# Kernel optimization log

Measured on AMD Instinct MI355X. Metric: run time of the kernel, lower is better.

Reference implementation:

```python
import jax, jax.numpy as jnp
import numpy as np

N, E, H, G = 50000, 800000, 256, 50
CUTOFF = 10.0
PI = float(np.pi)
LOG2 = float(np.log(2.0))

def ssp(x):
    # ShiftedSoftplus: softplus(x) - log(2)
    return jax.nn.softplus(x) - LOG2

def setup_inputs() -> dict:
    key = jax.random.key(0)
    ks = jax.random.split(key, 16)
    def lin(kw, kb, fan_in, fan_out):
        s = float(np.sqrt(6.0 / (fan_in + fan_out)))  # xavier_uniform
        W = jax.random.uniform(kw, (fan_in, fan_out), minval=-s, maxval=s, dtype=jnp.float32)
        b = jnp.zeros((fan_out,), jnp.float32)
        return W, b
    h = jax.random.normal(ks[0], (N, H), dtype=jnp.float32)
    edge_index = jax.random.randint(ks[1], (2, E), 0, N, dtype=jnp.int64)
    edge_weight = jax.random.uniform(ks[2], (E,), dtype=jnp.float32) * CUTOFF
    edge_attr = jax.random.normal(ks[3], (E, G), dtype=jnp.float32)
    aw_W, aw_b = lin(ks[4], ks[5], H, H)   # atom_wise
    m1_W, m1_b = lin(ks[6], ks[7], G, H)   # mlp[0]
    m2_W, m2_b = lin(ks[8], ks[9], H, H)   # mlp[2] (num_filters == hidden)
    o1_W, o1_b = lin(ks[10], ks[11], H, H) # out[0]
    o2_W, o2_b = lin(ks[12], ks[13], H, H) # out[2]
    return {"h": h, "edge_index": edge_index, "edge_weight": edge_weight,
            "edge_attr": edge_attr, "aw_W": aw_W, "aw_b": aw_b,
            "m1_W": m1_W, "m1_b": m1_b, "m2_W": m2_W, "m2_b": m2_b,
            "o1_W": o1_W, "o1_b": o1_b, "o2_W": o2_W, "o2_b": o2_b}

def reference(h, edge_index, edge_weight, edge_attr,
              aw_W, aw_b, m1_W, m1_b, m2_W, m2_b,
              o1_W, o1_b, o2_W, o2_b):
    n_nodes = h.shape[0]
    # atom-wise linear
    h1 = h @ aw_W + aw_b                                   # [N, H]
    # cosine cutoff per edge
    C = 0.5 * (jnp.cos(edge_weight * (PI / CUTOFF)) + 1.0) # [E]
    # edge filter MLP on RBF features
    Wf = ssp(ssp(edge_attr @ m1_W + m1_b) @ m2_W + m2_b)   # [E, H]
    Wf = Wf * C[:, None]
    # CFConv: gather x_j, modulate, scatter-add to target nodes
    src, dst = edge_index[0], edge_index[1]
    msg = h1[src] * Wf                                     # [E, H]
    agg = jax.ops.segment_sum(msg, dst, num_segments=n_nodes)
    # output MLP
    out = ssp(agg @ o1_W + o1_b) @ o2_W + o2_b             # [N, H]
    return out
```

## Files before the change

### kernel.cpp

```cpp
#include <hip/hip_runtime.h>

#define N_NODES 50000
#define N_EDGES 800000

typedef __attribute__((ext_vector_type(8))) short bf16x8;
typedef __attribute__((ext_vector_type(4))) float f32x4;
typedef __attribute__((ext_vector_type(2))) float f32x2;
typedef __attribute__((ext_vector_type(4))) unsigned int u32x4;

__device__ __forceinline__ float bf2f(unsigned int u) {
  union { unsigned int u; float f; } c; c.u = (u & 0xffffu) << 16; return c.f;
}
__device__ __forceinline__ unsigned short f2bf(float f) {
  union { float f; unsigned int u; } c; c.f = f;
  return (unsigned short)((c.u + 0x8000u) >> 16);
}
__device__ __forceinline__ unsigned int pk_bf16(float lo, float hi) {
  unsigned int r;
  asm("v_cvt_pk_bf16_f32 %0, %1, %2" : "=v"(r) : "v"(lo), "v"(hi));
  return r;
}

#if __has_builtin(__builtin_amdgcn_exp2f) && __has_builtin(__builtin_amdgcn_logf)
__device__ __forceinline__ float sspf(float x) {
  const float e = __builtin_amdgcn_exp2f(fabsf(x) * -1.44269504088896f);
  const float l = __builtin_amdgcn_logf(1.0f + e);
  return fmaf(0.69314718055994531f, l, fmaxf(x, 0.0f) - 0.69314718055994531f);
}
#else
__device__ __forceinline__ float sspf(float x) {
  return fmaxf(x, 0.0f) + __logf(1.0f + __expf(-fabsf(x))) - 0.69314718055994531f;
}
#endif

__device__ __forceinline__ f32x4 MFMA(bf16x8 a, bf16x8 b, f32x4 c) {
  return __builtin_amdgcn_mfma_f32_16x16x32_bf16(a, b, c, 0, 0, 0);
}
__device__ __forceinline__ f32x4 f4bcast(float v) {
  f32x4 z = {v, v, v, v}; return z;
}

__device__ __forceinline__ bf16x8 cvt8pk(const float* __restrict__ p) {
  f32x4 x0 = *(const f32x4*)p;
  f32x4 x1 = *(const f32x4*)(p + 4);
  union { u32x4 u; bf16x8 v; } r;
  r.u[0] = pk_bf16(x0[0], x0[1]);
  r.u[1] = pk_bf16(x0[2], x0[3]);
  r.u[2] = pk_bf16(x1[0], x1[1]);
  r.u[3] = pk_bf16(x1[2], x1[3]);
  return r.v;
}

template<int ADT, int ACT, int ODT>
__global__ __launch_bounds__(512, 8) void gemm512(
    const void* __restrict__ Av, const unsigned short* __restrict__ Wt,
    const float* __restrict__ bias, void* __restrict__ Outv, int M)
{
  __shared__ unsigned short a_lds[64 * 256];
  const int m0  = (int)blockIdx.x * 64;
  const int tid = (int)threadIdx.x;

  {
    const int r   = tid >> 3;
    const int oc8 = tid & 7;
    int row = m0 + r;
    if (row >= M) row = M - 1;
    if (ADT == 1) {
      const float* ap = (const float*)Av + (size_t)row * 256 + oc8 * 32;
#pragma unroll
      for (int q = 0; q < 4; ++q) {
        const bf16x8 v = cvt8pk(ap + q * 8);
        const int byt = r * 512 + ((oc8 * 64 + q * 16) ^ ((r & 7) << 4));
        *(bf16x8*)((char*)a_lds + byt) = v;
      }
    } else {
      const unsigned short* ap =
          (const unsigned short*)Av + (size_t)row * 256 + oc8 * 32;
#pragma unroll
      for (int q = 0; q < 4; ++q) {
        const bf16x8 v = *(const bf16x8*)(ap + q * 8);
        const int byt = r * 512 + ((oc8 * 64 + q * 16) ^ ((r & 7) << 4));
        *(bf16x8*)((char*)a_lds + byt) = v;
      }
    }
  }
  __syncthreads();

  const int w  = tid >> 6, l = tid & 63, lr = l & 15, g = l >> 4;
  const int c0 = w * 32;
  const int P45 = (lr & 3) << 4;
  const int P6  = (lr & 4) << 4;
  const int alb = lr * 512 + ((g * 16) ^ P45);

  const float bs0 = bias[c0 + lr];
  const float bs1 = bias[c0 + 16 + lr];
  f32x4 acc[4][2];
#pragma unroll
  for (int a = 0; a < 4; ++a) {
    acc[a][0] = f4bcast(bs0);
    acc[a][1] = f4bcast(bs1);
  }

#pragma unroll
  for (int ks = 0; ks < 8; ++ks) {
    const int kb = ks * 32 + g * 8;
    const bf16x8 bfr0 = *(const bf16x8*)(Wt + (size_t)(c0 + lr) * 256 + kb);
    const bf16x8 bfr1 = *(const bf16x8*)(Wt + (size_t)(c0 + 16 + lr) * 256 + kb);
    const char* abase = (const char*)a_lds + (alb + ((ks * 64) ^ P6));
#pragma unroll
    for (int mf = 0; mf < 4; ++mf) {
      const bf16x8 af = *(const bf16x8*)(abase + mf * 8192);
      __builtin_amdgcn_s_setprio(1);
      acc[mf][0] = MFMA(af, bfr0, acc[mf][0]);
      acc[mf][1] = MFMA(af, bfr1, acc[mf][1]);
      __builtin_amdgcn_s_setprio(0);
    }
  }

#pragma unroll
  for (int nf = 0; nf < 2; ++nf) {
    const int col = c0 + nf * 16 + lr;
#pragma unroll
    for (int mf = 0; mf < 4; ++mf) {
#pragma unroll
      for (int i = 0; i < 4; ++i) {
        const int row = m0 + mf * 16 + g * 4 + i;
        if (row < M) {
          float x = acc[mf][nf][i];
          if (ACT) x = sspf(x);
          if (ODT == 0)
            ((unsigned short*)Outv)[(size_t)row * 256 + col] = f2bf(x);
          else
            ((float*)Outv)[(size_t)row * 256 + col] = x;
        }
      }
    }
  }
}

__global__ __launch_bounds__(256) void hist_dst(const int* __restrict__ eidx,
                                                int* __restrict__ cnt)
{
  const int e = (int)blockIdx.x * 256 + (int)threadIdx.x;
  atomicAdd(&cnt[eidx[N_EDGES + e]], 1);
}

__global__ __launch_bounds__(1024) void scan_cnt(const int* __restrict__ cnt,
                                                 int* __restrict__ cursor)
{
  __shared__ int part[1024];
  const int t = (int)threadIdx.x;
  const int base = t * 49;
  int s = 0;
#pragma unroll 7
  for (int j = 0; j < 49; ++j) {
    const int idx = base + j;
    if (idx < N_NODES) s += cnt[idx];
  }
  part[t] = s;
  __syncthreads();
  for (int off = 1; off < 1024; off <<= 1) {
    int v = 0;
    if (t >= off) v = part[t - off];
    __syncthreads();
    part[t] += v;
    __syncthreads();
  }
  int run = (t == 0) ? 0 : part[t - 1];
#pragma unroll 7
  for (int j = 0; j < 49; ++j) {
    const int idx = base + j;
    if (idx < N_NODES) { cursor[idx] = run; run += cnt[idx]; }
  }
}

__global__ __launch_bounds__(256) void scatter_perm(
    const int* __restrict__ eidx, const float* __restrict__ ew,
    int* __restrict__ cursor, int* __restrict__ perm,
    float* __restrict__ Cf, int* __restrict__ srcs, int* __restrict__ dsts)
{
  const int e = (int)blockIdx.x * 256 + (int)threadIdx.x;
  const int d = eidx[N_EDGES + e];
  const int pos = atomicAdd(&cursor[d], 1);
  perm[pos] = e;
  Cf[pos]   = 0.5f * (__cosf(ew[e] * 0.31415926535897931f) + 1.0f);
  srcs[pos] = eidx[e];
  dsts[pos] = d;
}

__global__ __launch_bounds__(512, 8) void edge_fused512(
    const float* __restrict__ eattr, const int* __restrict__ perm,
    const float* __restrict__ Cf,
    const int* __restrict__ srcs, const int* __restrict__ dsts,
    const unsigned short* __restrict__ m1t, const float* __restrict__ m1b,
    const unsigned short* __restrict__ m2t, const float* __restrict__ m2b,
    const unsigned short* __restrict__ h1, float* __restrict__ agg)
{
  __shared__ unsigned short t_lds[64 * 256];
  __shared__ float Cs[64];
  __shared__ int s_src[64];
  __shared__ int s_dst[65];
  unsigned short* ea_lds = t_lds;

  const int e0  = (int)blockIdx.x * 64;
  const int tid = (int)threadIdx.x;

  {
    const int r  = tid >> 3;
    const int oc = tid & 7;
    const int p  = perm[e0 + r];
    const float* ap = eattr + (size_t)p * 50 + oc * 8;
    union { u32x4 u; bf16x8 v; } t;
    if (oc < 6) {
      f32x2 a0 = *(const f32x2*)(ap);
      f32x2 a1 = *(const f32x2*)(ap + 2);
      f32x2 a2 = *(const f32x2*)(ap + 4);
      f32x2 a3 = *(const f32x2*)(ap + 6);
      t.u[0] = pk_bf16(a0[0], a0[1]);
      t.u[1] = pk_bf16(a1[0], a1[1]);
      t.u[2] = pk_bf16(a2[0], a2[1]);
      t.u[3] = pk_bf16(a3[0], a3[1]);
    } else if (oc == 6) {
      f32x2 a0 = *(const f32x2*)(ap);
      t.u[0] = pk_bf16(a0[0], a0[1]);
      t.u[1] = 0; t.u[2] = 0; t.u[3] = 0;
    } else {
      t.u[0] = 0; t.u[1] = 0; t.u[2] = 0; t.u[3] = 0;
    }
    const int byt = r * 128 + ((oc * 16) ^ ((r & 7) << 4));
    *(bf16x8*)((char*)ea_lds + byt) = t.v;
  }
  if (tid < 64) {
    Cs[tid]    = Cf[e0 + tid];
    s_src[tid] = srcs[e0 + tid];
    s_dst[tid] = dsts[e0 + tid];
  }
  if (tid == 64)
    s_dst[64] = (e0 + 64 < N_EDGES) ? dsts[e0 + 64] : -1;
  __syncthreads();

  const int w  = tid >> 6;
  const int l  = tid & 63;
  const int lr = l & 15;
  const int g  = l >> 4;
  const int c0 = w * 32;

  const int P45  = (lr & 3) << 4;
  const int P6   = (lr & 4) << 4;
  const int alb1 = lr * 128 + ((g * 16) ^ P45);
  const int alb2 = lr * 512 + ((g * 16) ^ P45);

  const float b10 = m1b[c0 + lr];
  const float b11 = m1b[c0 + 16 + lr];
  f32x4 acc[4][2];
#pragma unroll
  for (int a = 0; a < 4; ++a) {
    acc[a][0] = f4bcast(b10);
    acc[a][1] = f4bcast(b11);
  }

#pragma unroll
  for (int ks = 0; ks < 2; ++ks) {
    const int kb = ks * 32 + g * 8;
    const bf16x8 bfr0 = *(const bf16x8*)(m1t + (c0 + lr) * 64 + kb);
    const bf16x8 bfr1 = *(const bf16x8*)(m1t + (c0 + 16 + lr) * 64 + kb);
    const char* abase = (const char*)ea_lds + (alb1 + ((ks * 64) ^ P6));
#pragma unroll
    for (int mf = 0; mf < 4; ++mf) {
      const bf16x8 af = *(const bf16x8*)(abase + mf * 2048);
      __builtin_amdgcn_s_setprio(1);
      acc[mf][0] = MFMA(af, bfr0, acc[mf][0]);
      acc[mf][1] = MFMA(af, bfr1, acc[mf][1]);
      __builtin_amdgcn_s_setprio(0);
    }
  }
  __syncthreads();

#pragma unroll
  for (int nf = 0; nf < 2; ++nf) {
    const int colb = (c0 + nf * 16 + lr) * 2;
#pragma unroll
    for (int i = 0; i < 4; ++i) {
      const int gi = g * 4 + i;
      char* wp = (char*)t_lds + (gi * 512 + (colb ^ ((gi & 7) << 4)));
      const float v0 = sspf(acc[0][nf][i]);
      const float v1 = sspf(acc[1][nf][i]);
      const float v2 = sspf(acc[2][nf][i]);
      const float v3 = sspf(acc[3][nf][i]);
      const unsigned int p01 = pk_bf16(v0, v1);
      const unsigned int p23 = pk_bf16(v2, v3);
      *(unsigned short*)(wp)         = (unsigned short)p01;
      *(unsigned short*)(wp + 8192)  = (unsigned short)(p01 >> 16);
      *(unsigned short*)(wp + 16384) = (unsigned short)p23;
      *(unsigned short*)(wp + 24576) = (unsigned short)(p23 >> 16);
    }
  }
  __syncthreads();

  const float b20 = m2b[c0 + lr];
  const float b21 = m2b[c0 + 16 + lr];
#pragma unroll
  for (int a = 0; a < 4; ++a) {
    acc[a][0] = f4bcast(b20);
    acc[a][1] = f4bcast(b21);
  }

#pragma unroll
  for (int ks = 0; ks < 8; ++ks) {
    const int kb = ks * 32 + g * 8;
    const bf16x8 bfr0 = *(const bf16x8*)(m2t + (size_t)(c0 + lr) * 256 + kb);
    const bf16x8 bfr1 = *(const bf16x8*)(m2t + (size_t)(c0 + 16 + lr) * 256 + kb);
    const char* abase = (const char*)t_lds + (alb2 + ((ks * 64) ^ P6));
#pragma unroll
    for (int mf = 0; mf < 4; ++mf) {
      const bf16x8 af = *(const bf16x8*)(abase + mf * 8192);
      __builtin_amdgcn_s_setprio(1);
      acc[mf][0] = MFMA(af, bfr0, acc[mf][0]);
      acc[mf][1] = MFMA(af, bfr1, acc[mf][1]);
      __builtin_amdgcn_s_setprio(0);
    }
  }
  __syncthreads();

#pragma unroll
  for (int nf = 0; nf < 2; ++nf) {
    const int colb = (c0 + nf * 16 + lr) * 2;
#pragma unroll
    for (int i = 0; i < 4; ++i) {
      const int gi = g * 4 + i;
      char* wp = (char*)t_lds + (gi * 512 + (colb ^ ((gi & 7) << 4)));
      const float v0 = sspf(acc[0][nf][i]) * Cs[gi];
      const float v1 = sspf(acc[1][nf][i]) * Cs[16 + gi];
      const float v2 = sspf(acc[2][nf][i]) * Cs[32 + gi];
      const float v3 = sspf(acc[3][nf][i]) * Cs[48 + gi];
      const unsigned int p01 = pk_bf16(v0, v1);
      const unsigned int p23 = pk_bf16(v2, v3);
      *(unsigned short*)(wp)         = (unsigned short)p01;
      *(unsigned short*)(wp + 8192)  = (unsigned short)(p01 >> 16);
      *(unsigned short*)(wp + 16384) = (unsigned short)p23;
      *(unsigned short*)(wp + 24576) = (unsigned short)(p23 >> 16);
    }
  }
  __syncthreads();

  {
    const int q2 = tid >> 7;
    const int cp = (tid & 127) * 2;
    const int rb = q2 * 16;
    float s0 = 0.f, s1 = 0.f;
#pragma unroll
    for (int rr = 0; rr < 16; ++rr) {
      const int r = rb + rr;
      const int byt = r * 512 + ((cp * 2) ^ ((r & 7) << 4));
      const unsigned int wfp = *(const unsigned int*)((const char*)t_lds + byt);
      const unsigned int xjp =
          *(const unsigned int*)(h1 + (size_t)s_src[r] * 256 + cp);
      s0 += bf2f(wfp) * bf2f(xjp);
      s1 += bf2f(wfp >> 16) * bf2f(xjp >> 16);
      const int d = s_dst[r];
      if (rr == 15 || s_dst[r + 1] != d) {
        float* ap = agg + (size_t)d * 256 + cp;
        atomicAdd(ap, s0);
        atomicAdd(ap + 1, s1);
        s0 = 0.f; s1 = 0.f;
      }
    }
  }
}

__global__ __launch_bounds__(256) void prep_weights(
    const float* __restrict__ aw, const float* __restrict__ m1,
    const float* __restrict__ m2, const float* __restrict__ o1,
    const float* __restrict__ o2,
    unsigned short* __restrict__ awt, unsigned short* __restrict__ m1t,
    unsigned short* __restrict__ m2t, unsigned short* __restrict__ o1t,
    unsigned short* __restrict__ o2t)
{
  const int i = (int)blockIdx.x * 256 + (int)threadIdx.x;
  const int c = i >> 8, k = i & 255;
  const int src = k * 256 + c;
  awt[i] = f2bf(aw[src]);
  m2t[i] = f2bf(m2[src]);
  o1t[i] = f2bf(o1[src]);
  o2t[i] = f2bf(o2[src]);
  if (k < 64) m1t[c * 64 + k] = (k < 50) ? f2bf(m1[k * 256 + c]) : (unsigned short)0;
}

extern "C" void kernel_launch(void* const* d_in, const int* in_sizes, int n_in,
                              void* d_out, int out_size, void* d_ws, size_t ws_size,
                              hipStream_t stream)
{
  const float* h    = (const float*)d_in[0];
  const int*   eidx = (const int*)d_in[1];
  const float* ew   = (const float*)d_in[2];
  const float* ea   = (const float*)d_in[3];
  const float* awW  = (const float*)d_in[4];
  const float* awb  = (const float*)d_in[5];
  const float* m1W  = (const float*)d_in[6];
  const float* m1b  = (const float*)d_in[7];
  const float* m2W  = (const float*)d_in[8];
  const float* m2b  = (const float*)d_in[9];
  const float* o1W  = (const float*)d_in[10];
  const float* o1b  = (const float*)d_in[11];
  const float* o2W  = (const float*)d_in[12];
  const float* o2b  = (const float*)d_in[13];

  char* ws = (char*)d_ws;
  unsigned short* h1  = (unsigned short*)ws;
  float*          agg = (float*)(ws + 25600000);
  char* wbase = ws + 25600000 + 51200000;
  unsigned short* awt = (unsigned short*)wbase;
  unsigned short* m2t = awt + 65536;
  unsigned short* o1t = m2t + 65536;
  unsigned short* o2t = o1t + 65536;
  unsigned short* m1t = o2t + 65536;
  char* p0 = wbase + 4 * 131072 + 32768;
  int* cnt    = (int*)p0;
  int* cursor = cnt + N_NODES;
  int* perm   = cursor + N_NODES;
  char* p1 = p0 + 400000 + 3200000;
  float* Cf   = (float*)p1;
  int*   srcs = (int*)(p1 + 3200000);
  int*   dsts = (int*)(p1 + 6400000);

  hipMemsetAsync(agg, 0, (size_t)N_NODES * 256 * 4, stream);
  hipMemsetAsync(cnt, 0, (size_t)N_NODES * 4, stream);

  prep_weights<<<256, 256, 0, stream>>>(awW, m1W, m2W, o1W, o2W,
                                        awt, m1t, m2t, o1t, o2t);
  hist_dst<<<N_EDGES / 256, 256, 0, stream>>>(eidx, cnt);
  scan_cnt<<<1, 1024, 0, stream>>>(cnt, cursor);
  scatter_perm<<<N_EDGES / 256, 256, 0, stream>>>(eidx, ew, cursor, perm,
                                                  Cf, srcs, dsts);

  gemm512<1, 0, 0><<<(N_NODES + 63) / 64, 512, 0, stream>>>(h, awt, awb, h1, N_NODES);

  edge_fused512<<<N_EDGES / 64, 512, 0, stream>>>(
      ea, perm, Cf, srcs, dsts, m1t, m1b, m2t, m2b, h1, agg);

  gemm512<1, 1, 0><<<(N_NODES + 63) / 64, 512, 0, stream>>>(agg, o1t, o1b, h1, N_NODES);
  gemm512<0, 0, 1><<<(N_NODES + 63) / 64, 512, 0, stream>>>(h1, o2t, o2b, d_out, N_NODES);
}
```

Baseline: 698.6 us.

## Fuse output MLP GEMMs, prefetch gathered features, replace interior atomics with stores

Adds out_fused512, which runs both output linear layers in one kernel and keeps the SSP intermediate in LDS as bf16 instead of writing it to global memory. In the edge kernel, the h1 source-row gathers are issued before the barrier into registers so they overlap with the filter epilogue. Segment sums whose destination does not cross a 16-row group boundary are written with plain vector stores instead of atomics, since edges are sorted by destination. This relies on each destination's edges being contiguous and fully owned by one thread group; a destination spanning more than two groups could be written non-atomically and give wrong results.

New measurement: 813.1 us. 16.4% more time.

```diff
diff --git a/kernel.cpp b/kernel.cpp
--- a/kernel.cpp
+++ b/kernel.cpp
@@ -138,6 +138,126 @@
   }
 }
 
+__global__ __launch_bounds__(512, 8) void out_fused512(
+    const float* __restrict__ agg,
+    const unsigned short* __restrict__ o1t, const float* __restrict__ o1b,
+    const unsigned short* __restrict__ o2t, const float* __restrict__ o2b,
+    float* __restrict__ Out, int M)
+{
+  __shared__ unsigned short t_lds[64 * 256];
+  const int m0  = (int)blockIdx.x * 64;
+  const int tid = (int)threadIdx.x;
+
+  {
+    const int r   = tid >> 3;
+    const int oc8 = tid & 7;
+    int row = m0 + r;
+    if (row >= M) row = M - 1;
+    const float* ap = agg + (size_t)row * 256 + oc8 * 32;
+#pragma unroll
+    for (int q = 0; q < 4; ++q) {
+      const bf16x8 v = cvt8pk(ap + q * 8);
+      const int byt = r * 512 + ((oc8 * 64 + q * 16) ^ ((r & 7) << 4));
+      *(bf16x8*)((char*)t_lds + byt) = v;
+    }
+  }
+  __syncthreads();
+
+  const int w  = tid >> 6, l = tid & 63, lr = l & 15, g = l >> 4;
+  const int c0 = w * 32;
+  const int P45 = (lr & 3) << 4;
+  const int P6  = (lr & 4) << 4;
+  const int alb = lr * 512 + ((g * 16) ^ P45);
+
+  f32x4 acc[4][2];
+  {
+    const float b0 = o1b[c0 + lr];
+    const float b1 = o1b[c0 + 16 + lr];
+#pragma unroll
+    for (int a = 0; a < 4; ++a) {
+      acc[a][0] = f4bcast(b0);
+      acc[a][1] = f4bcast(b1);
+    }
+  }
+
+#pragma unroll
+  for (int ks = 0; ks < 8; ++ks) {
+    const int kb = ks * 32 + g * 8;
+    const bf16x8 bfr0 = *(const bf16x8*)(o1t + (size_t)(c0 + lr) * 256 + kb);
+    const bf16x8 bfr1 = *(const bf16x8*)(o1t + (size_t)(c0 + 16 + lr) * 256 + kb);
+    const char* abase = (const char*)t_lds + (alb + ((ks * 64) ^ P6));
+#pragma unroll
+    for (int mf = 0; mf < 4; ++mf) {
+      const bf16x8 af = *(const bf16x8*)(abase + mf * 8192);
+      __builtin_amdgcn_s_setprio(1);
+      acc[mf][0] = MFMA(af, bfr0, acc[mf][0]);
+      acc[mf][1] = MFMA(af, bfr1, acc[mf][1]);
+      __builtin_amdgcn_s_setprio(0);
+    }
+  }
+  __syncthreads();
+
+#pragma unroll
+  for (int nf = 0; nf < 2; ++nf) {
+    const int colb = (c0 + nf * 16 + lr) * 2;
+#pragma unroll
+    for (int i = 0; i < 4; ++i) {
+      const int gi = g * 4 + i;
+      char* wp = (char*)t_lds + (gi * 512 + (colb ^ ((gi & 7) << 4)));
+      const float v0 = sspf(acc[0][nf][i]);
+      const float v1 = sspf(acc[1][nf][i]);
+      const float v2 = sspf(acc[2][nf][i]);
+      const float v3 = sspf(acc[3][nf][i]);
+      const unsigned int p01 = pk_bf16(v0, v1);
+      const unsigned int p23 = pk_bf16(v2, v3);
+      *(unsigned short*)(wp)         = (unsigned short)p01;
+      *(unsigned short*)(wp + 8192)  = (unsigned short)(p01 >> 16);
+      *(unsigned short*)(wp + 16384) = (unsigned short)p23;
+      *(unsigned short*)(wp + 24576) = (unsigned short)(p23 >> 16);
+    }
+  }
+  __syncthreads();
+
+  {
+    const float b0 = o2b[c0 + lr];
+    const float b1 = o2b[c0 + 16 + lr];
+#pragma unroll
+    for (int a = 0; a < 4; ++a) {
+      acc[a][0] = f4bcast(b0);
+      acc[a][1] = f4bcast(b1);
+    }
+  }
+#pragma unroll
+  for (int ks = 0; ks < 8; ++ks) {
+    const int kb = ks * 32 + g * 8;
+    const bf16x8 bfr0 = *(const bf16x8*)(o2t + (size_t)(c0 + lr) * 256 + kb);
+    const bf16x8 bfr1 = *(const bf16x8*)(o2t + (size_t)(c0 + 16 + lr) * 256 + kb);
+    const char* abase = (const char*)t_lds + (alb + ((ks * 64) ^ P6));
+#pragma unroll
+    for (int mf = 0; mf < 4; ++mf) {
+      const bf16x8 af = *(const bf16x8*)(abase + mf * 8192);
+      __builtin_amdgcn_s_setprio(1);
+      acc[mf][0] = MFMA(af, bfr0, acc[mf][0]);
+      acc[mf][1] = MFMA(af, bfr1, acc[mf][1]);
+      __builtin_amdgcn_s_setprio(0);
+    }
+  }
+
+#pragma unroll
+  for (int nf = 0; nf < 2; ++nf) {
+    const int col = c0 + nf * 16 + lr;
+#pragma unroll
+    for (int mf = 0; mf < 4; ++mf) {
+#pragma unroll
+      for (int i = 0; i < 4; ++i) {
+        const int row = m0 + mf * 16 + g * 4 + i;
+        if (row < M)
+          Out[(size_t)row * 256 + col] = acc[mf][nf][i];
+      }
+    }
+  }
+}
+
 __global__ __launch_bounds__(256) void hist_dst(const int* __restrict__ eidx,
                                                 int* __restrict__ cnt)
 {
@@ -199,7 +319,7 @@
   __shared__ unsigned short t_lds[64 * 256];
   __shared__ float Cs[64];
   __shared__ int s_src[64];
-  __shared__ int s_dst[65];
+  __shared__ int s_dstX[66];
   unsigned short* ea_lds = t_lds;
 
   const int e0  = (int)blockIdx.x * 64;
@@ -231,12 +351,14 @@
     *(bf16x8*)((char*)ea_lds + byt) = t.v;
   }
   if (tid < 64) {
-    Cs[tid]    = Cf[e0 + tid];
-    s_src[tid] = srcs[e0 + tid];
-    s_dst[tid] = dsts[e0 + tid];
-  }
-  if (tid == 64)
-    s_dst[64] = (e0 + 64 < N_EDGES) ? dsts[e0 + 64] : -1;
+    Cs[tid]         = Cf[e0 + tid];
+    s_src[tid]      = srcs[e0 + tid];
+    s_dstX[tid + 1] = dsts[e0 + tid];
+  } else if (tid == 64) {
+    s_dstX[65] = (e0 + 64 < N_EDGES) ? dsts[e0 + 64] : -1;
+  } else if (tid == 65) {
+    s_dstX[0] = (e0 > 0) ? dsts[e0 - 1] : -1;
+  }
   __syncthreads();
 
   const int w  = tid >> 6;
@@ -320,6 +442,15 @@
       __builtin_amdgcn_s_setprio(0);
     }
   }
+
+  const int q2 = tid >> 7;
+  const int cp = (tid & 127) * 2;
+  const int rb = q2 * 16;
+  unsigned int xjv[16];
+#pragma unroll
+  for (int rr = 0; rr < 16; ++rr)
+    xjv[rr] = *(const unsigned int*)(h1 + (size_t)s_src[rb + rr] * 256 + cp);
+
   __syncthreads();
 
 #pragma unroll
@@ -344,25 +475,28 @@
   __syncthreads();
 
   {
-    const int q2 = tid >> 7;
-    const int cp = (tid & 127) * 2;
-    const int rb = q2 * 16;
     float s0 = 0.f, s1 = 0.f;
+    int atHead = 1;
 #pragma unroll
     for (int rr = 0; rr < 16; ++rr) {
       const int r = rb + rr;
       const int byt = r * 512 + ((cp * 2) ^ ((r & 7) << 4));
       const unsigned int wfp = *(const unsigned int*)((const char*)t_lds + byt);
-      const unsigned int xjp =
-          *(const unsigned int*)(h1 + (size_t)s_src[r] * 256 + cp);
-      s0 += bf2f(wfp) * bf2f(xjp);
-      s1 += bf2f(wfp >> 16) * bf2f(xjp >> 16);
-      const int d = s_dst[r];
-      if (rr == 15 || s_dst[r + 1] != d) {
+      s0 += bf2f(wfp) * bf2f(xjv[rr]);
+      s1 += bf2f(wfp >> 16) * bf2f(xjv[rr] >> 16);
+      const int d = s_dstX[r + 1];
+      if (rr == 15 || s_dstX[r + 2] != d) {
+        const bool shared = (atHead && s_dstX[rb] == d) ||
+                            (rr == 15 && s_dstX[rb + 17] == d);
         float* ap = agg + (size_t)d * 256 + cp;
-        atomicAdd(ap, s0);
-        atomicAdd(ap + 1, s1);
-        s0 = 0.f; s1 = 0.f;
+        if (shared) {
+          atomicAdd(ap, s0);
+          atomicAdd(ap + 1, s1);
+        } else {
+          f32x2 v; v[0] = s0; v[1] = s1;
+          *(f32x2*)ap = v;
+        }
+        s0 = 0.f; s1 = 0.f; atHead = 0;
       }
     }
   }
@@ -438,6 +572,6 @@
   edge_fused512<<<N_EDGES / 64, 512, 0, stream>>>(
       ea, perm, Cf, srcs, dsts, m1t, m1b, m2t, m2b, h1, agg);
 
-  gemm512<1, 1, 0><<<(N_NODES + 63) / 64, 512, 0, stream>>>(agg, o1t, o1b, h1, N_NODES);
-  gemm512<0, 0, 1><<<(N_NODES + 63) / 64, 512, 0, stream>>>(h1, o2t, o2b, d_out, N_NODES);
-}
+  out_fused512<<<(N_NODES + 63) / 64, 512, 0, stream>>>(
+      agg, o1t, o1b, o2t, o2b, (float*)d_out, N_NODES);
+}
```
